# Optimization experiments

Measured on AMD Instinct MI355X. Metric: run time of the kernel, lower is better.

The kernel has to match this reference:

```python
import jax, jax.numpy as jnp
import numpy as np

L, N, EMB, H = 4, 50000, 128, 4
R, HID, LBL = 16, 64, 32
E = 625000


def setup_inputs() -> dict:
    key = jax.random.key(0)
    ks = jax.random.split(key, 10)
    s = 0.05
    return {
        "embedding": jax.random.normal(ks[0], (L, N, EMB), jnp.float32),
        "in_proj_w": jax.random.normal(ks[1], (3 * EMB, EMB), jnp.float32) * s,
        "in_proj_b": jnp.zeros((3 * EMB,), jnp.float32),
        "out_proj_w": jax.random.normal(ks[2], (EMB, EMB), jnp.float32) * s,
        "out_proj_b": jnp.zeros((EMB,), jnp.float32),
        "w1": jax.random.normal(ks[3], (R, EMB, HID), jnp.float32) * s,
        "root1": jax.random.normal(ks[4], (EMB, HID), jnp.float32) * s,
        "b1": jnp.zeros((HID,), jnp.float32),
        "w2": jax.random.normal(ks[5], (R, HID, LBL), jnp.float32) * s,
        "root2": jax.random.normal(ks[6], (HID, LBL), jnp.float32) * s,
        "b2": jnp.zeros((LBL,), jnp.float32),
        "edge_index": jax.random.randint(ks[7], (2, E), 0, N, dtype=jnp.int64),
        "edge_type": jax.random.randint(ks[8], (E,), 0, R, dtype=jnp.int64),
    }


def mha_self(x, wi, bi, wo, bo):
    # x: (L, N, EMB) -- torch nn.MultiheadAttention, batch_first=False, q=k=v=x
    Ls, Ns, Es = x.shape
    hd = Es // H
    qkv = x @ wi.T + bi                      # (L, N, 3E)
    q, k, v = jnp.split(qkv, 3, axis=-1)
    q = q.reshape(Ls, Ns, H, hd)
    k = k.reshape(Ls, Ns, H, hd)
    v = v.reshape(Ls, Ns, H, hd)
    scores = jnp.einsum('lnhd,mnhd->nhlm', q, k) / np.sqrt(hd).astype(np.float32)
    attn = jax.nn.softmax(scores, axis=-1)
    out = jnp.einsum('nhlm,mnhd->lnhd', attn, v).reshape(Ls, Ns, Es)
    return out @ wo.T + bo


def rgcn_layer(x, src, dst, etype, W, root, bias):
    # PyG RGCNConv (num_bases=None, aggr='mean'):
    # out[n] = x[n] @ root + bias + sum_r mean_{e: dst=n, type=r} x[src_e] @ W[r]
    Rr, fin, fout = W.shape
    seg = etype * N + dst                                   # (E,) combined (rel, dst)
    msg_sum = jax.ops.segment_sum(x[src], seg, num_segments=Rr * N)   # (R*N, fin)
    cnt = jax.ops.segment_sum(jnp.ones((src.shape[0],), x.dtype), seg,
                              num_segments=Rr * N)
    mean = (msg_sum / jnp.maximum(cnt, 1.0)[:, None]).reshape(Rr, N, fin)
    agg = jnp.einsum('rni,rio->no', mean, W)                # per-relation GEMM
    return agg + x @ root + bias


def reference(embedding, in_proj_w, in_proj_b, out_proj_w, out_proj_b,
              w1, root1, b1, w2, root2, b2, edge_index, edge_type):
    attn_out = mha_self(embedding, in_proj_w, in_proj_b, out_proj_w, out_proj_b)
    x = attn_out[0]                                         # (N, EMB)
    src, dst = edge_index[0], edge_index[1]
    x = jax.nn.relu(rgcn_layer(x, src, dst, edge_type, w1, root1, b1))
    x = rgcn_layer(x, src, dst, edge_type, w2, root2, b2)
    return jax.nn.softmax(x, axis=-1)
```

## Files before the change

### kernel.cpp

```cpp
#include <hip/hip_runtime.h>
#include <hip/hip_bf16.h>
#include <math.h>

#define NNODES 50000
#define NEDGE 625000
#define RREL 16
#define SCAN_NB 196

typedef __attribute__((ext_vector_type(8))) short short8;
typedef __attribute__((ext_vector_type(4))) float f32x4;

__device__ __forceinline__ float bfu(ushort u) {
  return __uint_as_float(((unsigned)u) << 16);
}
__device__ __forceinline__ ushort f2b(float f) {
  __hip_bfloat16 h = __float2bfloat16(f);
  return *(ushort*)&h;
}

__global__ __launch_bounds__(256) void prep_weights(
    const float* __restrict__ ipw, const float* __restrict__ opw,
    const float* __restrict__ w1, const float* __restrict__ root1,
    const float* __restrict__ w2, const float* __restrict__ root2,
    __hip_bfloat16* __restrict__ BTqkv, __hip_bfloat16* __restrict__ BTout,
    __hip_bfloat16* __restrict__ BT1, __hip_bfloat16* __restrict__ BT2) {
  int i = blockIdx.x * 256 + threadIdx.x;
  if (i < 49152) {
    BTqkv[i] = __float2bfloat16(ipw[i]);
  } else if (i < 65536) {
    int j = i - 49152;
    BTout[j] = __float2bfloat16(opw[j]);
  } else if (i < 65536 + 139264) {
    int j = i - 65536; int c = j / 128, k = j % 128;
    float v;
    if (c < 64) v = root1[k * 64 + c];
    else { int r = (c - 64) >> 6, o = (c - 64) & 63; v = w1[r * 8192 + k * 64 + o]; }
    BT1[j] = __float2bfloat16(v);
  } else if (i < 65536 + 139264 + 34816) {
    int j = i - 65536 - 139264; int c = j / 64, k = j % 64;
    float v;
    if (c < 32) v = root2[k * 32 + c];
    else { int r = (c - 32) >> 5, o = (c - 32) & 31; v = w2[r * 2048 + k * 32 + o]; }
    BT2[j] = __float2bfloat16(v);
  }
}

#define EPILOGUE_STORE(MEFF, NCOLS, LDC, BIASEXPR)                              \
  for (int p = 0; p < 2; p++) {                                                 \
    __syncthreads();                                                            \
    if ((w >> 1) == p) {                                                        \
      _Pragma("unroll")                                                         \
      for (int j = 0; j < 4; j++) {                                             \
        int coll = wc + j * 16 + lrow;                                          \
        float bv = (BIASEXPR);                                                  \
        _Pragma("unroll")                                                       \
        for (int i = 0; i < 4; i++) {                                           \
          int rloc = i * 16 + lk * 4;                                           \
          _Pragma("unroll")                                                     \
          for (int q = 0; q < 4; q++)                                           \
            Cs[(rloc + q) * 132 + coll] = f2b(acc[i][j][q] + bv);               \
        }                                                                       \
      }                                                                         \
    }                                                                           \
    __syncthreads();                                                            \
    _Pragma("unroll")                                                           \
    for (int idx = t; idx < 64 * 16; idx += 256) {                              \
      int r = idx >> 4, k = idx & 15;                                           \
      long gm = row0 + p * 64 + r;                                              \
      int col = col0 + k * 8;                                                   \
      if (gm < (MEFF) && col < (NCOLS))                                         \
        *(int4*)((ushort*)C + gm * (LDC) + col) = *(const int4*)(Cs + r * 132 + k * 8); \
    }                                                                           \
  }

__global__ __launch_bounds__(256) void qkv_gemm(
    const float* __restrict__ A, const __hip_bfloat16* __restrict__ BT,
    const float* __restrict__ bias, __hip_bfloat16* __restrict__ C) {
  __shared__ ushort As[128 * 128];
  __shared__ ushort Cs[64 * 132];
  const int t = threadIdx.x;
  const long row0 = (long)blockIdx.x * 128;

#pragma unroll
  for (int c = t; c < 128 * 16; c += 256) {
    int r = c >> 4, cc = c & 15;
    long gm = row0 + r;
    int4 v = make_int4(0, 0, 0, 0);
    if (gm < 200000) {
      const float* ap = A + gm * 128 + cc * 8;
      float4 f0 = *(const float4*)ap;
      float4 f1 = *(const float4*)(ap + 4);
      v.x = (int)f2b(f0.x) | ((int)f2b(f0.y) << 16);
      v.y = (int)f2b(f0.z) | ((int)f2b(f0.w) << 16);
      v.z = (int)f2b(f1.x) | ((int)f2b(f1.y) << 16);
      v.w = (int)f2b(f1.z) | ((int)f2b(f1.w) << 16);
    }
    *(int4*)(As + r * 128 + ((cc ^ (r & 7)) * 8)) = v;
  }
  __syncthreads();

  const int lane = t & 63, w = t >> 6;
  const int wr = (w >> 1) * 64, wc = (w & 1) * 64;
  const int lrow = lane & 15, lk = lane >> 4;
  const int nstrips = (row0 < NNODES) ? 3 : 2;

  for (int s = 0; s < nstrips; s++) {
    const int col0 = (s == 2) ? 0 : 128 + s * 128;
    const long Meff = (s == 2) ? NNODES : 200000;

    const ushort* bp[4];
#pragma unroll
    for (int j = 0; j < 4; j++)
      bp[j] = (const ushort*)BT + (long)(col0 + wc + j * 16 + lrow) * 128 + lk * 8;

    f32x4 acc[4][4];
#pragma unroll
    for (int i = 0; i < 4; i++)
#pragma unroll
      for (int j = 0; j < 4; j++) acc[i][j] = (f32x4){0.f, 0.f, 0.f, 0.f};

#pragma unroll
    for (int k0 = 0; k0 < 128; k0 += 32) {
      const int cb = k0 / 8 + lk;
      short8 af[4], bfr[4];
#pragma unroll
      for (int j = 0; j < 4; j++) bfr[j] = *(const short8*)(bp[j] + k0);
#pragma unroll
      for (int i = 0; i < 4; i++) {
        int ra = wr + i * 16 + lrow;
        af[i] = *(const short8*)(As + ra * 128 + ((cb ^ (ra & 7)) * 8));
      }
#pragma unroll
      for (int i = 0; i < 4; i++)
#pragma unroll
        for (int j = 0; j < 4; j++)
          acc[i][j] = __builtin_amdgcn_mfma_f32_16x16x32_bf16(af[i], bfr[j], acc[i][j], 0, 0, 0);
    }

    EPILOGUE_STORE(Meff, 384, 384, bias[col0 + coll])
  }
}

template <int K>
__global__ __launch_bounds__(256) void gemm_strips(
    const __hip_bfloat16* __restrict__ Av, const __hip_bfloat16* __restrict__ BT,
    const float* __restrict__ bias, __hip_bfloat16* __restrict__ C,
    int M, int N, int ldc, int spg) {
  constexpr int CPR = K / 8;
  __shared__ ushort As[128 * K];
  __shared__ ushort Cs[64 * 132];
  const int t = threadIdx.x;
  const long row0 = (long)blockIdx.x * 128;

#pragma unroll
  for (int c = t; c < 128 * CPR; c += 256) {
    int r = c / CPR, cc = c % CPR;
    long gm = row0 + r;
    int4 v = make_int4(0, 0, 0, 0);
    if (gm < M) v = *(const int4*)((const ushort*)Av + gm * K + cc * 8);
    *(int4*)(As + r * K + ((cc ^ (r & 7)) * 8)) = v;
  }
  __syncthreads();

  const int lane = t & 63, w = t >> 6;
  const int wr = (w >> 1) * 64, wc = (w & 1) * 64;
  const int lrow = lane & 15, lk = lane >> 4;
  const int nstrips = (N + 127) / 128;
  const int sbeg = blockIdx.y * spg;
  const int send = min(sbeg + spg, nstrips);

  for (int s = sbeg; s < send; s++) {
    const int col0 = s * 128;

    const ushort* bp[4];
#pragma unroll
    for (int j = 0; j < 4; j++) {
      int gn = col0 + wc + j * 16 + lrow;
      if (gn > N - 1) gn = N - 1;
      bp[j] = (const ushort*)BT + (long)gn * K + lk * 8;
    }

    f32x4 acc[4][4];
#pragma unroll
    for (int i = 0; i < 4; i++)
#pragma unroll
      for (int j = 0; j < 4; j++) acc[i][j] = (f32x4){0.f, 0.f, 0.f, 0.f};

#pragma unroll
    for (int k0 = 0; k0 < K; k0 += 32) {
      const int cb = k0 / 8 + lk;
      short8 af[4], bfr[4];
#pragma unroll
      for (int j = 0; j < 4; j++) bfr[j] = *(const short8*)(bp[j] + k0);
#pragma unroll
      for (int i = 0; i < 4; i++) {
        int ra = wr + i * 16 + lrow;
        af[i] = *(const short8*)(As + ra * K + ((cb ^ (ra & 7)) * 8));
      }
#pragma unroll
      for (int i = 0; i < 4; i++)
#pragma unroll
        for (int j = 0; j < 4; j++)
          acc[i][j] = __builtin_amdgcn_mfma_f32_16x16x32_bf16(af[i], bfr[j], acc[i][j], 0, 0, 0);
    }

    EPILOGUE_STORE(M, N, ldc, bias ? bias[min(col0 + coll, N - 1)] : 0.f)
  }
}

__global__ __launch_bounds__(256) void attn_kernel(
    const __hip_bfloat16* __restrict__ qkv, __hip_bfloat16* __restrict__ o0) {
  int w = threadIdx.x >> 6, lane = threadIdx.x & 63;
  int n = blockIdx.x * 4 + w;
  const ushort* base = (const ushort*)qkv;
  uint qv = *(const uint*)(base + (size_t)n * 384 + lane * 2);
  float q0 = bfu(qv & 0xffff), q1 = bfu(qv >> 16);
  float s[4];
#pragma unroll
  for (int m = 0; m < 4; m++) {
    uint kk = *(const uint*)(base + (size_t)(m * NNODES + n) * 384 + 128 + lane * 2);
    float p = q0 * bfu(kk & 0xffff) + q1 * bfu(kk >> 16);
#pragma unroll
    for (int off = 8; off; off >>= 1) p += __shfl_xor(p, off);
    s[m] = p * 0.17677669529663687f;
  }
  float mx = fmaxf(fmaxf(s[0], s[1]), fmaxf(s[2], s[3]));
  float e[4], sum = 0.f;
#pragma unroll
  for (int m = 0; m < 4; m++) { e[m] = __expf(s[m] - mx); sum += e[m]; }
  float inv = 1.0f / sum;
  float o0f = 0.f, o1f = 0.f;
#pragma unroll
  for (int m = 0; m < 4; m++) {
    uint vv = *(const uint*)(base + (size_t)(m * NNODES + n) * 384 + 256 + lane * 2);
    float wgt = e[m] * inv;
    o0f += wgt * bfu(vv & 0xffff);
    o1f += wgt * bfu(vv >> 16);
  }
  *(uint*)((ushort*)o0 + (size_t)n * 128 + lane * 2) = (uint)f2b(o0f) | ((uint)f2b(o1f) << 16);
}

__global__ __launch_bounds__(256) void count_edges(
    const int* __restrict__ dst, const int* __restrict__ et, int* __restrict__ cnt) {
  int e = blockIdx.x * 256 + threadIdx.x;
  if (e < NEDGE) atomicAdd(&cnt[et[e] * NNODES + dst[e]], 1);
}

__global__ __launch_bounds__(256) void scan1(
    const int* __restrict__ cnt, int* __restrict__ off, int* __restrict__ part) {
  int t = threadIdx.x, b = blockIdx.x;
  int i = b * 256 + t;
  int v = 0;
  if (i < NNODES) {
#pragma unroll
    for (int r = 0; r < RREL; r++) v += cnt[r * NNODES + i];
  }
  __shared__ int sm[256];
  sm[t] = v;
  __syncthreads();
#pragma unroll
  for (int o = 1; o < 256; o <<= 1) {
    int x = (t >= o) ? sm[t - o] : 0;
    __syncthreads();
    sm[t] += x;
    __syncthreads();
  }
  if (i < NNODES) off[i] = sm[t] - v;
  if (t == 255) part[b] = sm[t];
}

__global__ __launch_bounds__(256) void scan2(int* __restrict__ part) {
  int t = threadIdx.x;
  int v = (t < SCAN_NB) ? part[t] : 0;
  __shared__ int sm[256];
  sm[t] = v;
  __syncthreads();
#pragma unroll
  for (int o = 1; o < 256; o <<= 1) {
    int x = (t >= o) ? sm[t - o] : 0;
    __syncthreads();
    sm[t] += x;
    __syncthreads();
  }
  if (t < SCAN_NB) part[t] = sm[t] - v;
}

__global__ __launch_bounds__(256) void scan3(int* __restrict__ off, const int* __restrict__ part) {
  int i = blockIdx.x * 256 + threadIdx.x;
  if (i < NNODES) off[i] += part[blockIdx.x];
  if (i == 0) off[NNODES] = NEDGE;
}

__global__ __launch_bounds__(256) void scatter_edges(
    const int* __restrict__ src, const int* __restrict__ dst, const int* __restrict__ et,
    const int* __restrict__ cnt, const int* __restrict__ off,
    int* __restrict__ fill, unsigned* __restrict__ sorted, float* __restrict__ scales) {
  int e = blockIdx.x * 256 + threadIdx.x;
  if (e >= NEDGE) return;
  int d = dst[e], r = et[e], s = src[e];
  int pos = off[d] + atomicAdd(&fill[d], 1);
  sorted[pos] = (unsigned)s | ((unsigned)r << 16);
  scales[pos] = 1.0f / (float)cnt[r * NNODES + d];
}

__global__ __launch_bounds__(256) void fused1(
    const int* __restrict__ off, const unsigned* __restrict__ sorted,
    const float* __restrict__ scales, const ushort* __restrict__ Y1,
    const float* __restrict__ b1, __hip_bfloat16* __restrict__ x1b) {
  int w = threadIdx.x >> 6, lane = threadIdx.x & 63;
  int d = blockIdx.x * 4 + w;
  int s0 = off[d], s1 = off[d + 1];
  float acc = bfu(Y1[(size_t)d * 1088 + lane]) + b1[lane];
  for (int i = s0; i < s1; i++) {
    unsigned p = sorted[i];
    acc += bfu(Y1[(size_t)(p & 0xFFFF) * 1088 + 64 + (p >> 16) * 64 + lane]) * scales[i];
  }
  x1b[(size_t)d * 64 + lane] = __float2bfloat16(fmaxf(acc, 0.f));
}

__global__ __launch_bounds__(256) void fused2(
    const int* __restrict__ off, const unsigned* __restrict__ sorted,
    const float* __restrict__ scales, const ushort* __restrict__ Y2,
    const float* __restrict__ b2, float* __restrict__ out) {
  int w = threadIdx.x >> 6, lane = threadIdx.x & 63;
  int d = blockIdx.x * 4 + w;
  int j = lane & 31, half = lane >> 5;
  int s0 = off[d], s1 = off[d + 1];
  float acc = 0.f;
  for (int i = s0 + half; i < s1; i += 2) {
    unsigned p = sorted[i];
    acc += bfu(Y2[(size_t)(p & 0xFFFF) * 544 + 32 + (p >> 16) * 32 + j]) * scales[i];
  }
  acc += __shfl_xor(acc, 32);
  float v = acc + bfu(Y2[(size_t)d * 544 + j]) + b2[j];
  float mx = v;
#pragma unroll
  for (int o = 16; o; o >>= 1) mx = fmaxf(mx, __shfl_xor(mx, o));
  float e = __expf(v - mx);
  float sum = e;
#pragma unroll
  for (int o = 16; o; o >>= 1) sum += __shfl_xor(sum, o);
  if (half == 0) out[(size_t)d * 32 + j] = e / sum;
}

extern "C" void kernel_launch(void* const* d_in, const int* in_sizes, int n_in,
                              void* d_out, int out_size, void* d_ws, size_t ws_size,
                              hipStream_t stream) {
  (void)in_sizes; (void)n_in; (void)out_size; (void)ws_size;
  const float* emb   = (const float*)d_in[0];
  const float* ipw   = (const float*)d_in[1];
  const float* ipb   = (const float*)d_in[2];
  const float* opw   = (const float*)d_in[3];
  const float* opb   = (const float*)d_in[4];
  const float* w1    = (const float*)d_in[5];
  const float* root1 = (const float*)d_in[6];
  const float* b1    = (const float*)d_in[7];
  const float* w2    = (const float*)d_in[8];
  const float* root2 = (const float*)d_in[9];
  const float* b2    = (const float*)d_in[10];
  const int*   eidx  = (const int*)d_in[11];
  const int*   etype = (const int*)d_in[12];
  const int* srcp = eidx;
  const int* dstp = eidx + NEDGE;

  unsigned char* ws = (unsigned char*)d_ws;
  size_t off_b = 0;
  auto alloc = [&](size_t bytes) {
    unsigned char* p = ws + off_b;
    off_b += (bytes + 255) & ~(size_t)255;
    return p;
  };

  unsigned char* R = alloc(153600000);
  __hip_bfloat16* qkv = (__hip_bfloat16*)R;
  __hip_bfloat16* Y1  = (__hip_bfloat16*)R;
  __hip_bfloat16* Y2  = (__hip_bfloat16*)R;
  __hip_bfloat16* o0  = (__hip_bfloat16*)alloc(12800000);
  __hip_bfloat16* x0  = (__hip_bfloat16*)alloc(12800000);
  __hip_bfloat16* x1b = (__hip_bfloat16*)alloc(6400000);
  int*            cnt = (int*)alloc(3200000);
  int*            offs = (int*)alloc((NNODES + 1) * 4);
  int*            fill = (int*)alloc(NNODES * 4);
  int*            part = (int*)alloc(SCAN_NB * 4);
  unsigned*       sorted = (unsigned*)alloc(NEDGE * 4);
  float*          scales = (float*)alloc(NEDGE * 4);
  __hip_bfloat16* BTqkv = (__hip_bfloat16*)alloc(98304);
  __hip_bfloat16* BTout = (__hip_bfloat16*)alloc(32768);
  __hip_bfloat16* BT1   = (__hip_bfloat16*)alloc(278528);
  __hip_bfloat16* BT2   = (__hip_bfloat16*)alloc(69632);

  prep_weights<<<dim3((241664 + 255) / 256), dim3(256), 0, stream>>>(
      ipw, opw, w1, root1, w2, root2, BTqkv, BTout, BT1, BT2);
  hipMemsetAsync(cnt, 0, (size_t)RREL * NNODES * sizeof(int), stream);
  hipMemsetAsync(fill, 0, (size_t)NNODES * sizeof(int), stream);
  count_edges<<<dim3((NEDGE + 255) / 256), dim3(256), 0, stream>>>(dstp, etype, cnt);
  scan1<<<dim3(SCAN_NB), dim3(256), 0, stream>>>(cnt, offs, part);
  scan2<<<dim3(1), dim3(256), 0, stream>>>(part);
  scan3<<<dim3(SCAN_NB), dim3(256), 0, stream>>>(offs, part);
  scatter_edges<<<dim3((NEDGE + 255) / 256), dim3(256), 0, stream>>>(
      srcp, dstp, etype, cnt, offs, fill, sorted, scales);

  qkv_gemm<<<dim3(1563), dim3(256), 0, stream>>>(emb, BTqkv, ipb, qkv);

  attn_kernel<<<dim3(12500), dim3(256), 0, stream>>>(qkv, o0);

  gemm_strips<128><<<dim3(391, 1), dim3(256), 0, stream>>>(
      o0, BTout, opb, x0, NNODES, 128, 128, 1);

  gemm_strips<128><<<dim3(391, 3), dim3(256), 0, stream>>>(
      x0, BT1, nullptr, Y1, NNODES, 1088, 1088, 3);

  fused1<<<dim3(NNODES / 4), dim3(256), 0, stream>>>(
      offs, sorted, scales, (const ushort*)Y1, b1, x1b);

  gemm_strips<64><<<dim3(391, 2), dim3(256), 0, stream>>>(
      x1b, BT2, nullptr, Y2, NNODES, 544, 544, 3);

  fused2<<<dim3(NNODES / 4), dim3(256), 0, stream>>>(
      offs, sorted, scales, (const ushort*)Y2, b2, (float*)d_out);
}
```

Before: 385.4 us.

## Fold attention out-projection into RGCN layer-1 weights and unroll gather loops

Precomputes a combined weight matrix (out_proj composed with root1/W1) and a matching bias, so the separate out-projection GEMM over all nodes and its intermediate buffer are dropped. The layer-1 GEMM now reads the attention output directly. The qkv GEMM epilogue stages a full 128-row tile in shared memory in one pass instead of two, and both edge-gather kernels use multiple independent accumulators to raise memory-level parallelism. Folding the weights adds an extra bf16 rounding step on the combined weights, which slightly changes numerics.

```diff
diff --git a/kernel.cpp b/kernel.cpp
--- a/kernel.cpp
+++ b/kernel.cpp
@@ -22,14 +22,14 @@
     const float* __restrict__ ipw, const float* __restrict__ opw,
     const float* __restrict__ w1, const float* __restrict__ root1,
     const float* __restrict__ w2, const float* __restrict__ root2,
-    __hip_bfloat16* __restrict__ BTqkv, __hip_bfloat16* __restrict__ BTout,
+    __hip_bfloat16* __restrict__ BTqkv, __hip_bfloat16* __restrict__ BToutT,
     __hip_bfloat16* __restrict__ BT1, __hip_bfloat16* __restrict__ BT2) {
   int i = blockIdx.x * 256 + threadIdx.x;
   if (i < 49152) {
     BTqkv[i] = __float2bfloat16(ipw[i]);
   } else if (i < 65536) {
-    int j = i - 49152;
-    BTout[j] = __float2bfloat16(opw[j]);
+    int j = i - 49152; int m = j / 128, c = j % 128;
+    BToutT[j] = __float2bfloat16(opw[c * 128 + m]);
   } else if (i < 65536 + 139264) {
     int j = i - 65536; int c = j / 128, k = j % 128;
     float v;
@@ -42,6 +42,109 @@
     if (c < 32) v = root2[k * 32 + c];
     else { int r = (c - 32) >> 5, o = (c - 32) & 31; v = w2[r * 2048 + k * 32 + o]; }
     BT2[j] = __float2bfloat16(v);
+  }
+}
+
+__global__ __launch_bounds__(256) void prep_bias1(
+    const float* __restrict__ opb, const float* __restrict__ w1,
+    const float* __restrict__ root1, float* __restrict__ bias1) {
+  int j = blockIdx.x * 256 + threadIdx.x;
+  if (j >= 1088) return;
+  float s = 0.f;
+  if (j < 64) {
+    for (int c = 0; c < 128; c++) s += opb[c] * root1[c * 64 + j];
+  } else {
+    int r = (j - 64) >> 6, o = (j - 64) & 63;
+    for (int c = 0; c < 128; c++) s += opb[c] * w1[r * 8192 + c * 64 + o];
+  }
+  bias1[j] = s;
+}
+
+__global__ __launch_bounds__(256) void qkv_gemm(
+    const float* __restrict__ A, const __hip_bfloat16* __restrict__ BT,
+    const float* __restrict__ bias, __hip_bfloat16* __restrict__ C) {
+  __shared__ ushort As[128 * 128];
+  __shared__ ushort Cs[128 * 136];
+  const int t = threadIdx.x;
+  const long row0 = (long)blockIdx.x * 128;
+
+#pragma unroll
+  for (int c = t; c < 128 * 16; c += 256) {
+    int r = c >> 4, cc = c & 15;
+    long gm = row0 + r;
+    int4 v = make_int4(0, 0, 0, 0);
+    if (gm < 200000) {
+      const float* ap = A + gm * 128 + cc * 8;
+      float4 f0 = *(const float4*)ap;
+      float4 f1 = *(const float4*)(ap + 4);
+      v.x = (int)f2b(f0.x) | ((int)f2b(f0.y) << 16);
+      v.y = (int)f2b(f0.z) | ((int)f2b(f0.w) << 16);
+      v.z = (int)f2b(f1.x) | ((int)f2b(f1.y) << 16);
+      v.w = (int)f2b(f1.z) | ((int)f2b(f1.w) << 16);
+    }
+    *(int4*)(As + r * 128 + ((cc ^ (r & 7)) * 8)) = v;
+  }
+  __syncthreads();
+
+  const int lane = t & 63, w = t >> 6;
+  const int wr = (w >> 1) * 64, wc = (w & 1) * 64;
+  const int lrow = lane & 15, lk = lane >> 4;
+  const int nstrips = (row0 < NNODES) ? 3 : 2;
+
+  for (int s = 0; s < nstrips; s++) {
+    const int col0 = (s == 2) ? 0 : 128 + s * 128;
+    const long Meff = (s == 2) ? NNODES : 200000;
+
+    const ushort* bp[4];
+#pragma unroll
+    for (int j = 0; j < 4; j++)
+      bp[j] = (const ushort*)BT + (long)(col0 + wc + j * 16 + lrow) * 128 + lk * 8;
+
+    f32x4 acc[4][4];
+#pragma unroll
+    for (int i = 0; i < 4; i++)
+#pragma unroll
+      for (int j = 0; j < 4; j++) acc[i][j] = (f32x4){0.f, 0.f, 0.f, 0.f};
+
+#pragma unroll
+    for (int k0 = 0; k0 < 128; k0 += 32) {
+      const int cb = k0 / 8 + lk;
+      short8 af[4], bfr[4];
+#pragma unroll
+      for (int j = 0; j < 4; j++) bfr[j] = *(const short8*)(bp[j] + k0);
+#pragma unroll
+      for (int i = 0; i < 4; i++) {
+        int ra = wr + i * 16 + lrow;
+        af[i] = *(const short8*)(As + ra * 128 + ((cb ^ (ra & 7)) * 8));
+      }
+#pragma unroll
+      for (int i = 0; i < 4; i++)
+#pragma unroll
+        for (int j = 0; j < 4; j++)
+          acc[i][j] = __builtin_amdgcn_mfma_f32_16x16x32_bf16(af[i], bfr[j], acc[i][j], 0, 0, 0);
+    }
+
+    __syncthreads();
+#pragma unroll
+    for (int j = 0; j < 4; j++) {
+      int coll = wc + j * 16 + lrow;
+      float bv = bias[col0 + coll];
+#pragma unroll
+      for (int i = 0; i < 4; i++) {
+        int rbase = wr + i * 16 + lk * 4;
+#pragma unroll
+        for (int q = 0; q < 4; q++)
+          Cs[(rbase + q) * 136 + coll] = f2b(acc[i][j][q] + bv);
+      }
+    }
+    __syncthreads();
+#pragma unroll
+    for (int idx = t; idx < 128 * 16; idx += 256) {
+      int r = idx >> 4, k = idx & 15;
+      long gm = row0 + r;
+      if (gm < Meff)
+        *(int4*)((ushort*)C + gm * 384 + col0 + k * 8) = *(const int4*)(Cs + r * 136 + k * 8);
+    }
   }
 }
 
@@ -73,74 +176,6 @@
     }                                                                           \
   }
 
-__global__ __launch_bounds__(256) void qkv_gemm(
-    const float* __restrict__ A, const __hip_bfloat16* __restrict__ BT,
-    const float* __restrict__ bias, __hip_bfloat16* __restrict__ C) {
-  __shared__ ushort As[128 * 128];
-  __shared__ ushort Cs[64 * 132];
-  const int t = threadIdx.x;
-  const long row0 = (long)blockIdx.x * 128;
-
-#pragma unroll
-  for (int c = t; c < 128 * 16; c += 256) {
-    int r = c >> 4, cc = c & 15;
-    long gm = row0 + r;
-    int4 v = make_int4(0, 0, 0, 0);
-    if (gm < 200000) {
-      const float* ap = A + gm * 128 + cc * 8;
-      float4 f0 = *(const float4*)ap;
-      float4 f1 = *(const float4*)(ap + 4);
-      v.x = (int)f2b(f0.x) | ((int)f2b(f0.y) << 16);
-      v.y = (int)f2b(f0.z) | ((int)f2b(f0.w) << 16);
-      v.z = (int)f2b(f1.x) | ((int)f2b(f1.y) << 16);
-      v.w = (int)f2b(f1.z) | ((int)f2b(f1.w) << 16);
-    }
-    *(int4*)(As + r * 128 + ((cc ^ (r & 7)) * 8)) = v;
-  }
-  __syncthreads();
-
-  const int lane = t & 63, w = t >> 6;
-  const int wr = (w >> 1) * 64, wc = (w & 1) * 64;
-  const int lrow = lane & 15, lk = lane >> 4;
-  const int nstrips = (row0 < NNODES) ? 3 : 2;
-
-  for (int s = 0; s < nstrips; s++) {
-    const int col0 = (s == 2) ? 0 : 128 + s * 128;
-    const long Meff = (s == 2) ? NNODES : 200000;
-
-    const ushort* bp[4];
-#pragma unroll
-    for (int j = 0; j < 4; j++)
-      bp[j] = (const ushort*)BT + (long)(col0 + wc + j * 16 + lrow) * 128 + lk * 8;
-
-    f32x4 acc[4][4];
-#pragma unroll
-    for (int i = 0; i < 4; i++)
-#pragma unroll
-      for (int j = 0; j < 4; j++) acc[i][j] = (f32x4){0.f, 0.f, 0.f, 0.f};
-
-#pragma unroll
-    for (int k0 = 0; k0 < 128; k0 += 32) {
-      const int cb = k0 / 8 + lk;
-      short8 af[4], bfr[4];
-#pragma unroll
-      for (int j = 0; j < 4; j++) bfr[j] = *(const short8*)(bp[j] + k0);
-#pragma unroll
-      for (int i = 0; i < 4; i++) {
-        int ra = wr + i * 16 + lrow;
-        af[i] = *(const short8*)(As + ra * 128 + ((cb ^ (ra & 7)) * 8));
-      }
-#pragma unroll
-      for (int i = 0; i < 4; i++)
-#pragma unroll
-        for (int j = 0; j < 4; j++)
-          acc[i][j] = __builtin_amdgcn_mfma_f32_16x16x32_bf16(af[i], bfr[j], acc[i][j], 0, 0, 0);
-    }
-
-    EPILOGUE_STORE(Meff, 384, 384, bias[col0 + coll])
-  }
-}
-
 template <int K>
 __global__ __launch_bounds__(256) void gemm_strips(
     const __hip_bfloat16* __restrict__ Av, const __hip_bfloat16* __restrict__ BT,
@@ -310,11 +345,22 @@
   int w = threadIdx.x >> 6, lane = threadIdx.x & 63;
   int d = blockIdx.x * 4 + w;
   int s0 = off[d], s1 = off[d + 1];
-  float acc = bfu(Y1[(size_t)d * 1088 + lane]) + b1[lane];
-  for (int i = s0; i < s1; i++) {
+  float a0 = bfu(Y1[(size_t)d * 1088 + lane]) + b1[lane];
+  float a1 = 0.f, a2 = 0.f, a3 = 0.f;
+  int i = s0;
+  for (; i + 3 < s1; i += 4) {
+    unsigned p0 = sorted[i], p1 = sorted[i + 1], p2 = sorted[i + 2], p3 = sorted[i + 3];
+    float c0 = scales[i], c1 = scales[i + 1], c2 = scales[i + 2], c3 = scales[i + 3];
+    a0 += bfu(Y1[(size_t)(p0 & 0xFFFF) * 1088 + 64 + (p0 >> 16) * 64 + lane]) * c0;
+    a1 += bfu(Y1[(size_t)(p1 & 0xFFFF) * 1088 + 64 + (p1 >> 16) * 64 + lane]) * c1;
+    a2 += bfu(Y1[(size_t)(p2 & 0xFFFF) * 1088 + 64 + (p2 >> 16) * 64 + lane]) * c2;
+    a3 += bfu(Y1[(size_t)(p3 & 0xFFFF) * 1088 + 64 + (p3 >> 16) * 64 + lane]) * c3;
+  }
+  for (; i < s1; i++) {
     unsigned p = sorted[i];
-    acc += bfu(Y1[(size_t)(p & 0xFFFF) * 1088 + 64 + (p >> 16) * 64 + lane]) * scales[i];
-  }
+    a0 += bfu(Y1[(size_t)(p & 0xFFFF) * 1088 + 64 + (p >> 16) * 64 + lane]) * scales[i];
+  }
+  float acc = (a0 + a1) + (a2 + a3);
   x1b[(size_t)d * 64 + lane] = __float2bfloat16(fmaxf(acc, 0.f));
 }
 
@@ -326,11 +372,18 @@
   int d = blockIdx.x * 4 + w;
   int j = lane & 31, half = lane >> 5;
   int s0 = off[d], s1 = off[d + 1];
-  float acc = 0.f;
-  for (int i = s0 + half; i < s1; i += 2) {
+  float a0 = 0.f, a1 = 0.f;
+  int i = s0 + half;
+  for (; i + 2 < s1; i += 4) {
+    unsigned p0 = sorted[i], p1 = sorted[i + 2];
+    a0 += bfu(Y2[(size_t)(p0 & 0xFFFF) * 544 + 32 + (p0 >> 16) * 32 + j]) * scales[i];
+    a1 += bfu(Y2[(size_t)(p1 & 0xFFFF) * 544 + 32 + (p1 >> 16) * 32 + j]) * scales[i + 2];
+  }
+  for (; i < s1; i += 2) {
     unsigned p = sorted[i];
-    acc += bfu(Y2[(size_t)(p & 0xFFFF) * 544 + 32 + (p >> 16) * 32 + j]) * scales[i];
-  }
+    a0 += bfu(Y2[(size_t)(p & 0xFFFF) * 544 + 32 + (p >> 16) * 32 + j]) * scales[i];
+  }
+  float acc = a0 + a1;
   acc += __shfl_xor(acc, 32);
   float v = acc + bfu(Y2[(size_t)d * 544 + j]) + b2[j];
   float mx = v;
@@ -376,7 +429,6 @@
   __hip_bfloat16* Y1  = (__hip_bfloat16*)R;
   __hip_bfloat16* Y2  = (__hip_bfloat16*)R;
   __hip_bfloat16* o0  = (__hip_bfloat16*)alloc(12800000);
-  __hip_bfloat16* x0  = (__hip_bfloat16*)alloc(12800000);
   __hip_bfloat16* x1b = (__hip_bfloat16*)alloc(6400000);
   int*            cnt = (int*)alloc(3200000);
   int*            offs = (int*)alloc((NNODES + 1) * 4);
@@ -384,13 +436,16 @@
   int*            part = (int*)alloc(SCAN_NB * 4);
   unsigned*       sorted = (unsigned*)alloc(NEDGE * 4);
   float*          scales = (float*)alloc(NEDGE * 4);
-  __hip_bfloat16* BTqkv = (__hip_bfloat16*)alloc(98304);
-  __hip_bfloat16* BTout = (__hip_bfloat16*)alloc(32768);
-  __hip_bfloat16* BT1   = (__hip_bfloat16*)alloc(278528);
-  __hip_bfloat16* BT2   = (__hip_bfloat16*)alloc(69632);
+  __hip_bfloat16* BTqkv  = (__hip_bfloat16*)alloc(98304);
+  __hip_bfloat16* BToutT = (__hip_bfloat16*)alloc(32768);
+  __hip_bfloat16* BT1    = (__hip_bfloat16*)alloc(278528);
+  __hip_bfloat16* BT2    = (__hip_bfloat16*)alloc(69632);
+  __hip_bfloat16* BW     = (__hip_bfloat16*)alloc(278528);
+  float*          bias1  = (float*)alloc(4352);
 
   prep_weights<<<dim3((241664 + 255) / 256), dim3(256), 0, stream>>>(
-      ipw, opw, w1, root1, w2, root2, BTqkv, BTout, BT1, BT2);
+      ipw, opw, w1, root1, w2, root2, BTqkv, BToutT, BT1, BT2);
+  prep_bias1<<<dim3(5), dim3(256), 0, stream>>>(opb, w1, root1, bias1);
   hipMemsetAsync(cnt, 0, (size_t)RREL * NNODES * sizeof(int), stream);
   hipMemsetAsync(fill, 0, (size_t)NNODES * sizeof(int), stream);
   count_edges<<<dim3((NEDGE + 255) / 256), dim3(256), 0, stream>>>(dstp, etype, cnt);
@@ -400,15 +455,15 @@
   scatter_edges<<<dim3((NEDGE + 255) / 256), dim3(256), 0, stream>>>(
       srcp, dstp, etype, cnt, offs, fill, sorted, scales);
 
+  gemm_strips<128><<<dim3(9, 1), dim3(256), 0, stream>>>(
+      BT1, BToutT, nullptr, BW, 1088, 128, 128, 1);
+
   qkv_gemm<<<dim3(1563), dim3(256), 0, stream>>>(emb, BTqkv, ipb, qkv);
 
   attn_kernel<<<dim3(12500), dim3(256), 0, stream>>>(qkv, o0);
 
-  gemm_strips<128><<<dim3(391, 1), dim3(256), 0, stream>>>(
-      o0, BTout, opb, x0, NNODES, 128, 128, 1);
-
   gemm_strips<128><<<dim3(391, 3), dim3(256), 0, stream>>>(
-      x0, BT1, nullptr, Y1, NNODES, 1088, 1088, 3);
+      o0, BW, bias1, Y1, NNODES, 1088, 1088, 3);
 
   fused1<<<dim3(NNODES / 4), dim3(256), 0, stream>>>(
       offs, sorted, scales, (const ushort*)Y1, b1, x1b);
```

Result: faster. 340.2 us (-11.7%).
